# Performance work log

Hardware: AMD Instinct MI355X
Metric: run time of the kernel (lower is better)

The kernel has to match this reference:

```python
import jax, jax.numpy as jnp
import numpy as np

B, T, C = 4, 512, 1024          # batch, seq, n_embd
E, H = 8, 2048                  # n_total_experts, ffn hidden (ffn_factor*C)
N_SHARED, K = 1, 2              # shared experts, top-k routed
ROUTE_SCALE = 1.0


def setup_inputs() -> dict:
    key = jax.random.key(0)
    ks = jax.random.split(key, 6)
    s = 0.02
    return {
        "x": jax.random.normal(ks[0], (B, T, C), jnp.float32),
        "gate_w": jax.random.normal(ks[1], (C, E), jnp.float32) * s,
        "gate_b": jnp.zeros((E,), jnp.float32),
        "w1": jax.random.normal(ks[2], (E, C, H), jnp.float32) * s,
        "b1": jnp.zeros((E, H), jnp.float32),
        "w2": jax.random.normal(ks[3], (E, H, C), jnp.float32) * s,
        "b2": jnp.zeros((E, C), jnp.float32),
        "w3": jax.random.normal(ks[4], (E, C, H), jnp.float32) * s,
        "b3": jnp.zeros((E, H), jnp.float32),
    }


def reference(x, gate_w, gate_b, w1, b1, w2, b2, w3, b3):
    Bs, Ts, Cs = x.shape
    N = Bs * Ts
    xf = x.reshape(N, Cs)

    # --- gating (softmax in fp32, as in the torch code) ---
    logits = xf @ gate_w + gate_b                       # [N, E]
    scores = jax.nn.softmax(logits.astype(jnp.float32), axis=-1).astype(logits.dtype)

    topk_vals, topk_idx = jax.lax.top_k(scores[:, N_SHARED:], K)   # routed experts
    shared_ix = jnp.broadcast_to(jnp.arange(N_SHARED), (N, N_SHARED))
    all_idx = jnp.concatenate([shared_ix, topk_idx + N_SHARED], axis=-1)  # [N, S+K]
    all_w = jnp.concatenate([scores[:, :N_SHARED], topk_vals], axis=-1) * ROUTE_SCALE

    # combine-weight matrix: each expert selected at most once per token
    rows = jnp.arange(N)[:, None]
    cw = jnp.zeros((N, E), x.dtype).at[rows, all_idx].add(all_w)  # [N, E]

    # --- per-expert SwiGLU MLP (vectorized over experts; zero cw masks out) ---
    a = jnp.einsum('nc,ech->neh', xf, w1) + b1          # [N, E, H]
    g = jnp.einsum('nc,ech->neh', xf, w3) + b3
    h = jax.nn.silu(g) * a
    out = jnp.einsum('neh,ehc,ne->nc', h, w2, cw) + cw @ b2  # weighted combine

    # --- balance loss ---
    flat_idx = all_idx.reshape(-1)
    usage = jnp.zeros((E,), jnp.float32).at[flat_idx].add(1.0)
    score_sum = jnp.zeros((E,), jnp.float32).at[flat_idx].add(all_w.reshape(-1).astype(jnp.float32))
    Kp = float(N_SHARED + K)
    bal_loss = jnp.sum((float(E) / (Kp * N)) * usage * (score_sum / N))

    return out.reshape(Bs, Ts, Cs), bal_loss
```

## Files before the change

kernel.cpp:

```cpp
#include <hip/hip_runtime.h>
#include <stdint.h>

#define N_TOK 2048
#define C_DIM 1024
#define H_DIM 2048
#define NE 8
#define NSLOT 3

#define BM 128
#define BN 128
#define BK 64
#define PGRID 1024

#define WS_COUNTS   0
#define WS_PLAN     256
#define WS_CW       (WS_PLAN + 1024)
#define WS_ROUTE    (WS_CW + N_TOK*NE*4)
#define WS_LISTS    (WS_ROUTE + N_TOK*4)
#define WS_XB       (WS_LISTS + NE*N_TOK*4)
#define WS_HBUF     (WS_XB + (size_t)N_TOK*C_DIM*2)
#define WS_OUTSLOT  (WS_HBUF + (size_t)N_TOK*NSLOT*H_DIM*2)
#define WS_WT1T     (WS_OUTSLOT + (size_t)N_TOK*NSLOT*C_DIM*2)
#define WS_WT3T     (WS_WT1T + (size_t)NE*H_DIM*C_DIM*2)
#define WS_WT2T     (WS_WT3T + (size_t)NE*H_DIM*C_DIM*2)

typedef short bf16x8 __attribute__((ext_vector_type(8)));
typedef float f32x4 __attribute__((ext_vector_type(4)));

union FragU { bf16x8 v; uint2 u2[2]; };

__device__ __forceinline__ unsigned short f2b(float f) {
    union { float f; uint32_t u; } v; v.f = f;
    return (unsigned short)((v.u + 0x7fffu + ((v.u >> 16) & 1u)) >> 16);
}
__device__ __forceinline__ float b2f(unsigned short s) {
    union { uint32_t u; float f; } v; v.u = ((uint32_t)s) << 16; return v.f;
}

__device__ __forceinline__ void gload16(const unsigned short* g, unsigned short* l) {
    __builtin_amdgcn_global_load_lds(
        (const __attribute__((address_space(1))) unsigned int*)g,
        (__attribute__((address_space(3))) unsigned int*)l, 16, 0, 0);
}

__device__ __forceinline__ void tcast256(
        const float* __restrict__ src, unsigned short* __restrict__ dtile0,
        int N, int NKT, int kt, int nBase, char* lb, int t) {
    uint32_t* L = (uint32_t*)lb;
    const int l = t & 63, w = t >> 6;
    const float* s = src + (size_t)(kt * 64) * N + nBase;
#pragma unroll 4
    for (int i = 0; i < 16; i++) {
        int k = w * 16 + i;
        float4 v = *(const float4*)(s + (size_t)k * N + 4 * l);
        uint2 p;
        p.x = (uint32_t)f2b(v.x) | ((uint32_t)f2b(v.y) << 16);
        p.y = (uint32_t)f2b(v.z) | ((uint32_t)f2b(v.w) << 16);
        *(uint2*)(L + k * 130 + 2 * l) = p;
    }
    __syncthreads();
    const int rn = t >> 3, cc = t & 7;
#pragma unroll
    for (int s2 = 0; s2 < 8; s2++) {
        int n = s2 * 32 + rn;
        int np = n >> 1, hi = (n & 1) * 16;
        uint32_t o[4];
#pragma unroll
        for (int u = 0; u < 4; u++) {
            uint32_t a = L[(cc * 8 + 2 * u) * 130 + np];
            uint32_t b = L[(cc * 8 + 2 * u + 1) * 130 + np];
            o[u] = ((a >> hi) & 0xffffu) | (((b >> hi) & 0xffffu) << 16);
        }
        unsigned short* drow = dtile0 + (size_t)s2 * NKT * 2048 + rn * 64 + cc * 8;
        *(uint4*)drow = *(uint4*)o;
    }
}

__global__ __launch_bounds__(256) void prep_kernel(
        const float* __restrict__ x, const float* __restrict__ gw,
        const float* __restrict__ gb, const float* __restrict__ w1,
        const float* __restrict__ w3, float* __restrict__ cw,
        unsigned short* __restrict__ xb, int* __restrict__ route,
        unsigned short* __restrict__ wt1t, unsigned short* __restrict__ wt3t) {
    __shared__ __align__(16) char smem[33792];
    const int b = blockIdx.x;
    if (b >= 512) {
        int bb = b - 512;
        int op = bb >> 10, r2 = bb & 1023;
        int e = r2 >> 7, rem = r2 & 127, kt = rem >> 3, nB = rem & 7;
        const float* src = (op ? w3 : w1) + (size_t)e * C_DIM * H_DIM;
        unsigned short* dst = (op ? wt3t : wt1t) +
                              ((size_t)(e * 64 + nB * 8) * 16 + kt) * 2048;
        tcast256(src, dst, H_DIM, 16, kt, nB * 256, smem, threadIdx.x);
        return;
    }
    int n = (b * 256 + threadIdx.x) >> 6;
    int lane = threadIdx.x & 63;
    float acc[NE];
#pragma unroll
    for (int e = 0; e < NE; e++) acc[e] = 0.f;
    for (int c = lane; c < C_DIM; c += 64) {
        float xv = x[n * C_DIM + c];
        xb[n * C_DIM + c] = f2b(xv);
        const float* g = gw + c * NE;
#pragma unroll
        for (int e = 0; e < NE; e++) acc[e] += xv * g[e];
    }
#pragma unroll
    for (int e = 0; e < NE; e++) {
#pragma unroll
        for (int off = 32; off >= 1; off >>= 1) acc[e] += __shfl_xor(acc[e], off, 64);
        acc[e] += gb[e];
    }
    float m = acc[0];
#pragma unroll
    for (int e = 1; e < NE; e++) m = fmaxf(m, acc[e]);
    float s = 0.f, sc[NE];
#pragma unroll
    for (int e = 0; e < NE; e++) { sc[e] = __expf(acc[e] - m); s += sc[e]; }
    float inv = 1.f / s;
#pragma unroll
    for (int e = 0; e < NE; e++) sc[e] *= inv;
    int i1 = 1; float v1 = sc[1];
#pragma unroll
    for (int e = 2; e < NE; e++) if (sc[e] > v1) { v1 = sc[e]; i1 = e; }
    int i2 = 0; float v2 = -1.f;
#pragma unroll
    for (int e = 1; e < NE; e++) if (e != i1 && sc[e] > v2) { v2 = sc[e]; i2 = e; }
    if (lane < NE) {
        float v = 0.f;
        if (lane == 0) v = sc[0];
        else if (lane == i1) v = v1;
        else if (lane == i2) v = v2;
        cw[n * NE + lane] = v;
    }
    if (lane == 0) route[n] = i1 | (i2 << 8);
}

__global__ void lists_kernel(const int* __restrict__ route, int* __restrict__ counts,
                             int* __restrict__ lists) {
    const int e = blockIdx.x, lane = threadIdx.x;
    if (e == 0) {
        for (int base = 0; base < N_TOK; base += 64)
            lists[base + lane] = (base + lane) * 4;
        if (lane == 0) counts[0] = N_TOK;
        return;
    }
    int cnt = 0;
    for (int base = 0; base < N_TOK; base += 64) {
        int r = route[base + lane];
        int i1 = r & 255, i2 = (r >> 8) & 255;
        bool mt = (i1 == e) || (i2 == e);
        int slot = (i1 == e) ? 1 : 2;
        unsigned long long mask = __ballot(mt);
        int pos = __popcll(mask & ((1ull << lane) - 1ull));
        if (mt) lists[e * N_TOK + cnt + pos] = (base + lane) * 4 + slot;
        cnt += __popcll(mask);
    }
    if (lane == 0) counts[e] = cnt;
}

__global__ void plan_kernel(const int* __restrict__ counts, int* __restrict__ plan) {
    if (threadIdx.x == 0) {
        int p = 0;
        for (int e = 0; e < NE; e++) {
            int nb = (counts[e] + BM - 1) / BM;
            for (int m = 0; m < nb; m++) plan[1 + p++] = (e << 8) | m;
        }
        plan[0] = p;
    }
}

#define STAGE(A_, B_, NA, NB, aoff, boff) do {                            \
    _Pragma("unroll")                                                     \
    for (int i_ = 0; i_ < (NA); i_++)                                     \
        gload16(asrc[i_] + (aoff), (A_) + (i_ * 256 + t) * 8);            \
    _Pragma("unroll")                                                     \
    for (int i_ = 0; i_ < (NB); i_++)                                     \
        gload16(bsrc[i_] + (boff), (B_) + (i_ * 256 + t) * 8);            \
} while (0)

#define COMPUTE(A_, B_, NT, BEXPR) do {                                   \
    __builtin_amdgcn_s_setprio(1);                                        \
    _Pragma("unroll")                                                     \
    for (int j_ = 0; j_ < 2; j_++) {                                      \
        FragU af[4], bf[NT];                                              \
        _Pragma("unroll")                                                 \
        for (int mt = 0; mt < 4; mt++) {                                  \
            int row = wr * 64 + mt * 16 + ln15;                           \
            int slot = (j_ * 4 + lg) ^ swz;                               \
            af[mt].v = *(const bf16x8*)((A_) + row * BK + slot * 8);      \
        }                                                                 \
        _Pragma("unroll")                                                 \
        for (int nt = 0; nt < (NT); nt++) {                               \
            int row = (BEXPR);                                            \
            int slot = (j_ * 4 + lg) ^ swz;                               \
            bf[nt].v = *(const bf16x8*)((B_) + row * BK + slot * 8);      \
        }                                                                 \
        _Pragma("unroll")                                                 \
        for (int mt = 0; mt < 4; mt++)                                    \
            _Pragma("unroll")                                             \
            for (int nt = 0; nt < (NT); nt++)                             \
                acc[mt][nt] = __builtin_amdgcn_mfma_f32_16x16x32_bf16(    \
                    af[mt].v, bf[nt].v, acc[mt][nt], 0, 0, 0);            \
    }                                                                     \
    __builtin_amdgcn_s_setprio(0);                                        \
} while (0)

#define KLOOP2(NK, NA, NB, NT, BEXPR) do {                                \
    STAGE(As0_, Bs0_, NA, NB, 0, 0);                                      \
    asm volatile("s_waitcnt vmcnt(0)" ::: "memory");                      \
    __builtin_amdgcn_s_barrier();                                         \
    for (int kt = 0; kt < (NK); kt += 2) {                                \
        STAGE(As1_, Bs1_, NA, NB, (kt + 1) * BK, (kt + 1) * 2048);        \
        COMPUTE(As0_, Bs0_, NT, BEXPR);                                   \
        asm volatile("s_waitcnt vmcnt(0)" ::: "memory");                  \
        __builtin_amdgcn_s_barrier();                                     \
        if (kt + 2 < (NK))                                                \
            STAGE(As0_, Bs0_, NA, NB, (kt + 2) * BK, (kt + 2) * 2048);    \
        COMPUTE(As1_, Bs1_, NT, BEXPR);                                   \
        asm volatile("s_waitcnt vmcnt(0)" ::: "memory");                  \
        __builtin_amdgcn_s_barrier();                                     \
    }                                                                     \
} while (0)

__global__ __launch_bounds__(256, 2) void expert_up_kernel(
        const unsigned short* __restrict__ xb, const unsigned short* __restrict__ wt1t,
        const unsigned short* __restrict__ wt3t, const float* __restrict__ b1,
        const float* __restrict__ b3, const int* __restrict__ counts,
        const int* __restrict__ lists, const int* __restrict__ plan,
        unsigned short* __restrict__ hbuf, const float* __restrict__ w2,
        unsigned short* __restrict__ wt2t) {
    const int t = threadIdx.x;
    const int lane = t & 63, w = t >> 6;
    const int ln15 = lane & 15, lg = lane >> 4;
    const int wr = w >> 1, wc = w & 1;
    const int swz = ln15 & 7;

    __shared__ __align__(16) char smem[66048];
    unsigned short* As0_ = (unsigned short*)smem;
    unsigned short* As1_ = (unsigned short*)(smem + 16384);
    unsigned short* Bs0_ = (unsigned short*)(smem + 32768);
    unsigned short* Bs1_ = (unsigned short*)(smem + 49152);
    int* rowtok = (int*)(smem + 65536);

    const int ntile = plan[0] << 5;
    for (int tile = blockIdx.x; tile < ntile; tile += PGRID) {
        const int mi = tile >> 5, nb = tile & 31;
        const int ent = plan[1 + mi];
        const int e = ent >> 8, m0 = (ent & 255) * BM;
        const int cnt = counts[e];

        if (t < BM) {
            int r = m0 + t;
            rowtok[t] = lists[e * N_TOK + (r < cnt ? r : cnt - 1)];
        }
        __syncthreads();

        const unsigned short* asrc[4];
        const unsigned short* bsrc[4];
#pragma unroll
        for (int i = 0; i < 4; i++) {
            int c = i * 256 + t;
            int row = c >> 3, kc = (c & 7) ^ (row & 7);
            asrc[i] = xb + (size_t)(rowtok[row] >> 2) * C_DIM + kc * 8;
        }
#pragma unroll
        for (int i = 0; i < 4; i++) {
            int c = i * 256 + t;
            int r = c >> 3, kc = (c & 7) ^ (r & 7);
            int g = r >> 4;
            const unsigned short* wb = (g & 1) ? wt3t : wt1t;
            int rb = nb * 2 + (g >> 2);
            int trow = ((g >> 1) & 1) * 16 + (r & 15);
            bsrc[i] = wb + ((size_t)(e * 64 + rb) * 16) * 2048 + trow * 64 + kc * 8;
        }

        f32x4 acc[4][4];
#pragma unroll
        for (int a = 0; a < 4; a++)
#pragma unroll
            for (int b = 0; b < 4; b++) acc[a][b] = (f32x4){0.f, 0.f, 0.f, 0.f};

        KLOOP2(C_DIM / BK, 4, 4, 4, wc * 64 + nt * 16 + ln15);

#pragma unroll
        for (int p = 0; p < 2; p++) {
            int h = nb * 64 + (wc * 2 + p) * 16 + ln15;
            float bb1 = b1[e * H_DIM + h], bb3 = b3[e * H_DIM + h];
#pragma unroll
            for (int mt = 0; mt < 4; mt++) {
#pragma unroll
                for (int jj = 0; jj < 4; jj++) {
                    int mrow = wr * 64 + mt * 16 + lg * 4 + jj;
                    float av = acc[mt][2 * p][jj] + bb1;
                    float gv = acc[mt][2 * p + 1][jj] + bb3;
                    float hv = av * gv / (1.f + __expf(-gv));
                    int ent2 = rowtok[mrow];
                    hbuf[(size_t)((ent2 >> 2) * NSLOT + (ent2 & 3)) * H_DIM + h] = f2b(hv);
                }
            }
        }
        __syncthreads();
    }

    {
        int bb = blockIdx.x;
        int e = bb >> 7, rem = bb & 127, kt = rem >> 2, nB = rem & 3;
        tcast256(w2 + (size_t)e * H_DIM * C_DIM,
                 wt2t + ((size_t)(e * 32 + nB * 8) * 32 + kt) * 2048,
                 C_DIM, 32, kt, nB * 256, smem, t);
    }
}

__global__ __launch_bounds__(256, 3) void expert_down_kernel(
        const unsigned short* __restrict__ hbuf, const unsigned short* __restrict__ wt2t,
        const float* __restrict__ b2, const float* __restrict__ cw,
        const int* __restrict__ counts, const int* __restrict__ lists,
        const int* __restrict__ plan, unsigned short* __restrict__ outslot) {
    const int t = threadIdx.x;
    const int lane = t & 63, w = t >> 6;
    const int ln15 = lane & 15, lg = lane >> 4;
    const int wr = w >> 1, wc = w & 1;
    const int swz = ln15 & 7;

    __shared__ __align__(16) char smem[49664];
    unsigned short* As0_ = (unsigned short*)smem;
    unsigned short* As1_ = (unsigned short*)(smem + 16384);
    unsigned short* Bs0_ = (unsigned short*)(smem + 32768);
    unsigned short* Bs1_ = (unsigned short*)(smem + 40960);
    int* rowtok = (int*)(smem + 49152);

    const int ntile = plan[0] << 4;
    for (int tile = blockIdx.x; tile < ntile; tile += PGRID) {
        const int mi = tile >> 4, nb = tile & 15;
        const int ent = plan[1 + mi];
        const int e = ent >> 8, m0 = (ent & 255) * BM;
        const int cnt = counts[e];
        const int c0 = nb * 64;

        if (t < BM) {
            int r = m0 + t;
            rowtok[t] = lists[e * N_TOK + (r < cnt ? r : cnt - 1)];
        }
        __syncthreads();

        const unsigned short* asrc[4];
        const unsigned short* bsrc[2];
#pragma unroll
        for (int i = 0; i < 4; i++) {
            int c = i * 256 + t;
            int row = c >> 3, kc = (c & 7) ^ (row & 7);
            int ent2 = rowtok[row];
            asrc[i] = hbuf + (size_t)((ent2 >> 2) * NSLOT + (ent2 & 3)) * H_DIM + kc * 8;
        }
#pragma unroll
        for (int i = 0; i < 2; i++) {
            int c = i * 256 + t;
            int row = c >> 3, kc = (c & 7) ^ (row & 7);
            bsrc[i] = wt2t + (size_t)(e * 32 + nb * 2 + (row >> 5)) * 32 * 2048 +
                      (size_t)(row & 31) * 64 + kc * 8;
        }

        f32x4 acc[4][2];
#pragma unroll
        for (int a = 0; a < 4; a++)
#pragma unroll
            for (int b = 0; b < 2; b++) acc[a][b] = (f32x4){0.f, 0.f, 0.f, 0.f};

        KLOOP2(H_DIM / BK, 4, 2, 2, wc * 32 + nt * 16 + ln15);

#pragma unroll
        for (int nt = 0; nt < 2; nt++) {
            int col = c0 + wc * 32 + nt * 16 + ln15;
            float bb = b2[e * C_DIM + col];
#pragma unroll
            for (int mt = 0; mt < 4; mt++) {
#pragma unroll
                for (int jj = 0; jj < 4; jj++) {
                    int mrow = wr * 64 + mt * 16 + lg * 4 + jj;
                    int ent2 = rowtok[mrow];
                    int tok = ent2 >> 2, slot = ent2 & 3;
                    float cwv = cw[tok * NE + e];
                    outslot[(size_t)(tok * NSLOT + slot) * C_DIM + col] =
                        f2b(cwv * (acc[mt][nt][jj] + bb));
                }
            }
        }
        __syncthreads();
    }
}

__global__ __launch_bounds__(256) void reduce_loss_kernel(
        const unsigned short* __restrict__ os, const float* __restrict__ cw,
        const int* __restrict__ counts, float* __restrict__ out) {
    if (blockIdx.x < 1024) {
        int i = blockIdx.x * 256 + threadIdx.x;
        int n = i >> 7;
        int c = (i & 127) * 8;
        const unsigned short* p0 = os + ((size_t)n * NSLOT + 0) * C_DIM + c;
        const unsigned short* p1 = os + ((size_t)n * NSLOT + 1) * C_DIM + c;
        const unsigned short* p2 = os + ((size_t)n * NSLOT + 2) * C_DIM + c;
        uint4 a = *(const uint4*)p0, b = *(const uint4*)p1, d = *(const uint4*)p2;
        const unsigned short* sa = (const unsigned short*)&a;
        const unsigned short* sb = (const unsigned short*)&b;
        const unsigned short* sd = (const unsigned short*)&d;
        float r[8];
#pragma unroll
        for (int j = 0; j < 8; j++) r[j] = b2f(sa[j]) + b2f(sb[j]) + b2f(sd[j]);
        float* o = out + (size_t)n * C_DIM + c;
        *(float4*)o = *(float4*)&r[0];
        *(float4*)(o + 4) = *(float4*)&r[4];
    } else if (threadIdx.x < 64) {
        int lane = threadIdx.x;
        float ss[NE];
#pragma unroll
        for (int e = 0; e < NE; e++) ss[e] = 0.f;
        for (int n = lane; n < N_TOK; n += 64) {
#pragma unroll
            for (int e = 0; e < NE; e++) ss[e] += cw[n * NE + e];
        }
#pragma unroll
        for (int e = 0; e < NE; e++) {
#pragma unroll
            for (int off = 32; off >= 1; off >>= 1) ss[e] += __shfl_xor(ss[e], off, 64);
        }
        if (lane == 0) {
            float bal = 0.f;
            const float fac = (float)NE / (3.f * (float)N_TOK * (float)N_TOK);
#pragma unroll
            for (int e = 0; e < NE; e++) bal += fac * (float)counts[e] * ss[e];
            out[(size_t)N_TOK * C_DIM] = bal;
        }
    }
}

extern "C" void kernel_launch(void* const* d_in, const int* in_sizes, int n_in,
                              void* d_out, int out_size, void* d_ws, size_t ws_size,
                              hipStream_t stream) {
    const float* x  = (const float*)d_in[0];
    const float* gw = (const float*)d_in[1];
    const float* gb = (const float*)d_in[2];
    const float* w1 = (const float*)d_in[3];
    const float* b1 = (const float*)d_in[4];
    const float* w2 = (const float*)d_in[5];
    const float* b2 = (const float*)d_in[6];
    const float* w3 = (const float*)d_in[7];
    const float* b3 = (const float*)d_in[8];
    float* out = (float*)d_out;
    char* ws = (char*)d_ws;
    int*            counts = (int*)(ws + WS_COUNTS);
    int*            plan   = (int*)(ws + WS_PLAN);
    float*          cw     = (float*)(ws + WS_CW);
    int*            route  = (int*)(ws + WS_ROUTE);
    int*            lists  = (int*)(ws + WS_LISTS);
    unsigned short* xb     = (unsigned short*)(ws + WS_XB);
    unsigned short* hbuf   = (unsigned short*)(ws + WS_HBUF);
    unsigned short* oslot  = (unsigned short*)(ws + WS_OUTSLOT);
    unsigned short* wt1t   = (unsigned short*)(ws + WS_WT1T);
    unsigned short* wt3t   = (unsigned short*)(ws + WS_WT3T);
    unsigned short* wt2t   = (unsigned short*)(ws + WS_WT2T);

    hipLaunchKernelGGL(prep_kernel, dim3(2560), dim3(256), 0, stream,
                       x, gw, gb, w1, w3, cw, xb, route, wt1t, wt3t);
    hipLaunchKernelGGL(lists_kernel, dim3(NE), dim3(64), 0, stream,
                       route, counts, lists);
    hipLaunchKernelGGL(plan_kernel, dim3(1), dim3(64), 0, stream, counts, plan);
    hipLaunchKernelGGL(expert_up_kernel, dim3(PGRID), dim3(256), 0, stream,
                       xb, wt1t, wt3t, b1, b3, counts, lists, plan, hbuf, w2, wt2t);
    hipLaunchKernelGGL(expert_down_kernel, dim3(PGRID), dim3(256), 0, stream,
                       hbuf, wt2t, b2, cw, counts, lists, plan, oslot);
    hipLaunchKernelGGL(reduce_loss_kernel, dim3(1025), dim3(256), 0, stream,
                       oslot, cw, counts, out);
}
```

Measured before the change: 200.2 us.

## Shrink up-projection N tile and overlap next-stage loads with compute

The up-projection kernel's N tile is halved (64 w1/w3 columns to 32 each), which halves its B shared-memory buffers and accumulators and raises launch bounds to 3 blocks per SM for more occupancy. The k-loop is restructured so the next stage's global loads are issued before waiting only on the previous stage (vmcnt(6)), letting loads overlap with MFMA compute in both the up and down kernels. The trade-off is that each A tile is now loaded twice as often relative to B, and more barriers are added per iteration.

```diff
diff --git a/kernel.cpp b/kernel.cpp
--- a/kernel.cpp
+++ b/kernel.cpp
@@ -8,7 +8,6 @@
 #define NSLOT 3
 
 #define BM 128
-#define BN 128
 #define BK 64
 #define PGRID 1024
 
@@ -171,20 +170,20 @@
     }
 }
 
-#define STAGE(A_, B_, NA, NB, aoff, boff) do {                            \
+#define STAGE(A_, B_, aoff, boff) do {                                    \
     _Pragma("unroll")                                                     \
-    for (int i_ = 0; i_ < (NA); i_++)                                     \
+    for (int i_ = 0; i_ < 4; i_++)                                        \
         gload16(asrc[i_] + (aoff), (A_) + (i_ * 256 + t) * 8);            \
     _Pragma("unroll")                                                     \
-    for (int i_ = 0; i_ < (NB); i_++)                                     \
+    for (int i_ = 0; i_ < 2; i_++)                                        \
         gload16(bsrc[i_] + (boff), (B_) + (i_ * 256 + t) * 8);            \
 } while (0)
 
-#define COMPUTE(A_, B_, NT, BEXPR) do {                                   \
+#define COMPUTE(A_, B_, BEXPR) do {                                       \
     __builtin_amdgcn_s_setprio(1);                                        \
     _Pragma("unroll")                                                     \
     for (int j_ = 0; j_ < 2; j_++) {                                      \
-        FragU af[4], bf[NT];                                              \
+        FragU af[4], bf[2];                                               \
         _Pragma("unroll")                                                 \
         for (int mt = 0; mt < 4; mt++) {                                  \
             int row = wr * 64 + mt * 16 + ln15;                           \
@@ -192,7 +191,7 @@
             af[mt].v = *(const bf16x8*)((A_) + row * BK + slot * 8);      \
         }                                                                 \
         _Pragma("unroll")                                                 \
-        for (int nt = 0; nt < (NT); nt++) {                               \
+        for (int nt = 0; nt < 2; nt++) {                                  \
             int row = (BEXPR);                                            \
             int slot = (j_ * 4 + lg) ^ swz;                               \
             bf[nt].v = *(const bf16x8*)((B_) + row * BK + slot * 8);      \
@@ -200,31 +199,34 @@
         _Pragma("unroll")                                                 \
         for (int mt = 0; mt < 4; mt++)                                    \
             _Pragma("unroll")                                             \
-            for (int nt = 0; nt < (NT); nt++)                             \
+            for (int nt = 0; nt < 2; nt++)                                \
                 acc[mt][nt] = __builtin_amdgcn_mfma_f32_16x16x32_bf16(    \
                     af[mt].v, bf[nt].v, acc[mt][nt], 0, 0, 0);            \
     }                                                                     \
     __builtin_amdgcn_s_setprio(0);                                        \
 } while (0)
 
-#define KLOOP2(NK, NA, NB, NT, BEXPR) do {                                \
-    STAGE(As0_, Bs0_, NA, NB, 0, 0);                                      \
-    asm volatile("s_waitcnt vmcnt(0)" ::: "memory");                      \
-    __builtin_amdgcn_s_barrier();                                         \
+#define KLOOPC(NK, BEXPR) do {                                            \
+    STAGE(As0_, Bs0_, 0, 0);                                              \
     for (int kt = 0; kt < (NK); kt += 2) {                                \
-        STAGE(As1_, Bs1_, NA, NB, (kt + 1) * BK, (kt + 1) * 2048);        \
-        COMPUTE(As0_, Bs0_, NT, BEXPR);                                   \
-        asm volatile("s_waitcnt vmcnt(0)" ::: "memory");                  \
+        STAGE(As1_, Bs1_, (kt + 1) * BK, (kt + 1) * 2048);                \
+        asm volatile("s_waitcnt vmcnt(6)" ::: "memory");                  \
         __builtin_amdgcn_s_barrier();                                     \
-        if (kt + 2 < (NK))                                                \
-            STAGE(As0_, Bs0_, NA, NB, (kt + 2) * BK, (kt + 2) * 2048);    \
-        COMPUTE(As1_, Bs1_, NT, BEXPR);                                   \
-        asm volatile("s_waitcnt vmcnt(0)" ::: "memory");                  \
+        COMPUTE(As0_, Bs0_, BEXPR);                                       \
+        __builtin_amdgcn_s_barrier();                                     \
+        if (kt + 2 < (NK)) {                                              \
+            STAGE(As0_, Bs0_, (kt + 2) * BK, (kt + 2) * 2048);            \
+            asm volatile("s_waitcnt vmcnt(6)" ::: "memory");              \
+        } else {                                                          \
+            asm volatile("s_waitcnt vmcnt(0)" ::: "memory");              \
+        }                                                                 \
+        __builtin_amdgcn_s_barrier();                                     \
+        COMPUTE(As1_, Bs1_, BEXPR);                                       \
         __builtin_amdgcn_s_barrier();                                     \
     }                                                                     \
 } while (0)
 
-__global__ __launch_bounds__(256, 2) void expert_up_kernel(
+__global__ __launch_bounds__(256, 3) void expert_up_kernel(
         const unsigned short* __restrict__ xb, const unsigned short* __restrict__ wt1t,
         const unsigned short* __restrict__ wt3t, const float* __restrict__ b1,
         const float* __restrict__ b3, const int* __restrict__ counts,
@@ -237,16 +239,16 @@
     const int wr = w >> 1, wc = w & 1;
     const int swz = ln15 & 7;
 
-    __shared__ __align__(16) char smem[66048];
+    __shared__ __align__(16) char smem[49664];
     unsigned short* As0_ = (unsigned short*)smem;
     unsigned short* As1_ = (unsigned short*)(smem + 16384);
     unsigned short* Bs0_ = (unsigned short*)(smem + 32768);
-    unsigned short* Bs1_ = (unsigned short*)(smem + 49152);
-    int* rowtok = (int*)(smem + 65536);
-
-    const int ntile = plan[0] << 5;
+    unsigned short* Bs1_ = (unsigned short*)(smem + 40960);
+    int* rowtok = (int*)(smem + 49152);
+
+    const int ntile = plan[0] << 6;
     for (int tile = blockIdx.x; tile < ntile; tile += PGRID) {
-        const int mi = tile >> 5, nb = tile & 31;
+        const int mi = tile >> 6, nb = tile & 63;
         const int ent = plan[1 + mi];
         const int e = ent >> 8, m0 = (ent & 255) * BM;
         const int cnt = counts[e];
@@ -257,8 +259,10 @@
         }
         __syncthreads();
 
+        const unsigned short* wb1 = wt1t + (size_t)(e * 64 + nb) * 16 * 2048;
+        const unsigned short* wb3 = wt3t + (size_t)(e * 64 + nb) * 16 * 2048;
         const unsigned short* asrc[4];
-        const unsigned short* bsrc[4];
+        const unsigned short* bsrc[2];
 #pragma unroll
         for (int i = 0; i < 4; i++) {
             int c = i * 256 + t;
@@ -266,35 +270,30 @@
             asrc[i] = xb + (size_t)(rowtok[row] >> 2) * C_DIM + kc * 8;
         }
 #pragma unroll
-        for (int i = 0; i < 4; i++) {
+        for (int i = 0; i < 2; i++) {
             int c = i * 256 + t;
-            int r = c >> 3, kc = (c & 7) ^ (r & 7);
-            int g = r >> 4;
-            const unsigned short* wb = (g & 1) ? wt3t : wt1t;
-            int rb = nb * 2 + (g >> 2);
-            int trow = ((g >> 1) & 1) * 16 + (r & 15);
-            bsrc[i] = wb + ((size_t)(e * 64 + rb) * 16) * 2048 + trow * 64 + kc * 8;
-        }
-
-        f32x4 acc[4][4];
+            int row = c >> 3, kc = (c & 7) ^ (row & 7);
+            bsrc[i] = (row < 32 ? wb1 : wb3) + (size_t)(row & 31) * 64 + kc * 8;
+        }
+
+        f32x4 acc[4][2];
 #pragma unroll
         for (int a = 0; a < 4; a++)
 #pragma unroll
-            for (int b = 0; b < 4; b++) acc[a][b] = (f32x4){0.f, 0.f, 0.f, 0.f};
-
-        KLOOP2(C_DIM / BK, 4, 4, 4, wc * 64 + nt * 16 + ln15);
-
-#pragma unroll
-        for (int p = 0; p < 2; p++) {
-            int h = nb * 64 + (wc * 2 + p) * 16 + ln15;
+            for (int b = 0; b < 2; b++) acc[a][b] = (f32x4){0.f, 0.f, 0.f, 0.f};
+
+        KLOOPC(C_DIM / BK, nt * 32 + wc * 16 + ln15);
+
+        {
+            int h = nb * 32 + wc * 16 + ln15;
             float bb1 = b1[e * H_DIM + h], bb3 = b3[e * H_DIM + h];
 #pragma unroll
             for (int mt = 0; mt < 4; mt++) {
 #pragma unroll
                 for (int jj = 0; jj < 4; jj++) {
                     int mrow = wr * 64 + mt * 16 + lg * 4 + jj;
-                    float av = acc[mt][2 * p][jj] + bb1;
-                    float gv = acc[mt][2 * p + 1][jj] + bb3;
+                    float av = acc[mt][0][jj] + bb1;
+                    float gv = acc[mt][1][jj] + bb3;
                     float hv = av * gv / (1.f + __expf(-gv));
                     int ent2 = rowtok[mrow];
                     hbuf[(size_t)((ent2 >> 2) * NSLOT + (ent2 & 3)) * H_DIM + h] = f2b(hv);
@@ -368,7 +367,7 @@
 #pragma unroll
             for (int b = 0; b < 2; b++) acc[a][b] = (f32x4){0.f, 0.f, 0.f, 0.f};
 
-        KLOOP2(H_DIM / BK, 4, 2, 2, wc * 32 + nt * 16 + ln15);
+        KLOOPC(H_DIM / BK, wc * 32 + nt * 16 + ln15);
 
 #pragma unroll
         for (int nt = 0; nt < 2; nt++) {
```

After: 211.9 us. +5.8%, slower.
